# Kernel optimization log

Hardware: AMD Instinct MI355X
Metric: run time of the kernel (lower is better)

## Reference

```python
import jax, jax.numpy as jnp
import numpy as np

B, IN, H = 8192, 1024, 1024


def setup_inputs() -> dict:
    key = jax.random.key(0)
    ks = jax.random.split(key, 20)
    std = 1.0 / np.sqrt(H)
    u = lambda k, shape: jax.random.uniform(k, shape, jnp.float32, -std, std)
    inp = {
        "x": jax.random.normal(ks[0], (B, IN), jnp.float32),
        "hx": jax.random.normal(ks[1], (B, H), jnp.float32),
        "cx": jax.random.normal(ks[2], (B, H), jnp.float32),
        "task_id": 0,
        # x2h weights [H, IN] (torch Linear layout) and biases [H]
        "wxi": u(ks[3], (H, IN)), "bxi": u(ks[4], (H,)),
        "wxf": u(ks[5], (H, IN)), "bxf": u(ks[6], (H,)),
        "wxc": u(ks[7], (H, IN)), "bxc": u(ks[8], (H,)),
        "wxo": u(ks[9], (H, IN)), "bxo": u(ks[10], (H,)),
        # h2h weights [H, H] and biases [H]
        "whi": u(ks[11], (H, H)), "bhi": u(ks[12], (H,)),
        "whf": u(ks[13], (H, H)), "bhf": u(ks[14], (H,)),
        "whc": u(ks[15], (H, H)), "bhc": u(ks[16], (H,)),
        "who": u(ks[17], (H, H)), "bho": u(ks[18], (H,)),
    }
    return inp


def reference(x, hx, cx, task_id,
              wxi, bxi, wxf, bxf, wxc, bxc, wxo, bxo,
              whi, bhi, whf, bhf, whc, bhc, who, bho):
    # x = x.view(-1, x.size(1)) is identity for 2D input
    # gate pre-activations: Linear(x) + Linear(hx)  (torch: x @ W.T + b)
    ingate = x @ wxi.T + bxi + hx @ whi.T + bhi
    forgetgate = x @ wxf.T + bxf + hx @ whf.T + bhf
    cellgate = x @ wxc.T + bxc + hx @ whc.T + bhc
    outgate = x @ wxo.T + bxo + hx @ who.T + bho

    i = jax.nn.sigmoid(ingate)
    f = jax.nn.sigmoid(forgetgate)
    g = jnp.tanh(cellgate)
    o = jax.nn.sigmoid(outgate)

    cy = cx * f + i * g
    hy = o * jnp.tanh(cy)
    return hy, cy
```

## Files before the change

### kernel.cpp

```cpp
#include <hip/hip_runtime.h>
#include <hip/hip_bf16.h>

#define B_DIM  8192
#define IN_DIM 1024
#define H_DIM  1024
#define K_DIM  2048
#define BK     64
#define NT     (K_DIM / BK)

typedef __attribute__((ext_vector_type(8))) short bf16x8;
typedef __attribute__((ext_vector_type(4))) float f32x4;

__device__ __forceinline__ void mfma_16x16x32_bf16(f32x4& d, const bf16x8& a, const bf16x8& b) {
  asm("v_mfma_f32_16x16x32_bf16 %0, %1, %2, %0" : "+v"(d) : "v"(a), "v"(b));
}

__device__ __forceinline__ void gload16(const void* g, void* l) {
  __builtin_amdgcn_global_load_lds(
      (const __attribute__((address_space(1))) void*)g,
      (__attribute__((address_space(3))) void*)l,
      16, 0, 0);
}

__device__ __forceinline__ float fast_sigmoid(float x) {
  return 1.0f / (1.0f + __expf(-x));
}
__device__ __forceinline__ float fast_tanh(float x) {
  float e = __expf(2.0f * x);
  return 1.0f - 2.0f / (e + 1.0f);
}

__global__ __launch_bounds__(256) void pack_a_kernel(
    const float* __restrict__ x, const float* __restrict__ hx,
    __hip_bfloat16* __restrict__ A) {
  const int idx = blockIdx.x * 256 + threadIdx.x;
  const int r  = idx >> 8;
  const int kk = (idx & 255) << 3;
  const float* src = (kk < IN_DIM) ? (x + (size_t)r * IN_DIM + kk)
                                   : (hx + (size_t)r * H_DIM + (kk - IN_DIM));
  const float4 v0 = ((const float4*)src)[0];
  const float4 v1 = ((const float4*)src)[1];
  __hip_bfloat16 t[8];
  t[0] = __float2bfloat16(v0.x); t[1] = __float2bfloat16(v0.y);
  t[2] = __float2bfloat16(v0.z); t[3] = __float2bfloat16(v0.w);
  t[4] = __float2bfloat16(v1.x); t[5] = __float2bfloat16(v1.y);
  t[6] = __float2bfloat16(v1.z); t[7] = __float2bfloat16(v1.w);
  *(uint4*)(A + ((size_t)idx << 3)) = *(const uint4*)t;
}

__global__ __launch_bounds__(256) void pack_w_kernel(
    const float* __restrict__ wxi, const float* __restrict__ wxf,
    const float* __restrict__ wxc, const float* __restrict__ wxo,
    const float* __restrict__ whi, const float* __restrict__ whf,
    const float* __restrict__ whc, const float* __restrict__ who,
    __hip_bfloat16* __restrict__ W) {
  const int idx = blockIdx.x * 256 + threadIdx.x;
  const int row = idx >> 8;
  const int kk  = (idx & 255) << 3;
  const int g = row >> 10, n = row & 1023;
  const float* src;
  if (kk < IN_DIM) {
    const float* p = (g == 0) ? wxi : (g == 1) ? wxf : (g == 2) ? wxc : wxo;
    src = p + (size_t)n * IN_DIM + kk;
  } else {
    const float* p = (g == 0) ? whi : (g == 1) ? whf : (g == 2) ? whc : who;
    src = p + (size_t)n * H_DIM + (kk - IN_DIM);
  }
  const float4 v0 = ((const float4*)src)[0];
  const float4 v1 = ((const float4*)src)[1];
  __hip_bfloat16 t[8];
  t[0] = __float2bfloat16(v0.x); t[1] = __float2bfloat16(v0.y);
  t[2] = __float2bfloat16(v0.z); t[3] = __float2bfloat16(v0.w);
  t[4] = __float2bfloat16(v1.x); t[5] = __float2bfloat16(v1.y);
  t[6] = __float2bfloat16(v1.z); t[7] = __float2bfloat16(v1.w);
  *(uint4*)(W + ((size_t)idx << 3)) = *(const uint4*)t;
}

__global__ __launch_bounds__(512, 2) void lstm_gemm_kernel(
    const __hip_bfloat16* __restrict__ A,
    const __hip_bfloat16* __restrict__ W,
    const float* __restrict__ cx,
    const float* __restrict__ bxi, const float* __restrict__ bhi,
    const float* __restrict__ bxf, const float* __restrict__ bhf,
    const float* __restrict__ bxc, const float* __restrict__ bhc,
    const float* __restrict__ bxo, const float* __restrict__ bho,
    float* __restrict__ hy, float* __restrict__ cy) {

  __shared__ __align__(16) char lds[2][64 * 1024];

  const int tid  = threadIdx.x;
  const int w    = tid >> 6;
  const int lane = tid & 63;
  const int wm = w >> 2, wn = w & 3;
  const int lq = lane >> 4, lr16 = lane & 15;

  const int bid = blockIdx.x;
  const int xcd = bid & 7, idx = bid >> 3;
  const int col_tile = xcd * 2 + (idx >> 5);
  const int row_tile = idx & 31;
  const int row0 = row_tile * 256;
  const int col0 = col_tile * 64;

  const int srow = tid >> 3;
  const int scs  = (tid & 7) ^ (srow & 7);
  const __hip_bfloat16* Asrc = A + (size_t)(row0 + srow) * K_DIM + scs * 8;
  const __hip_bfloat16* Wsrc = W + (size_t)(col0 + srow) * K_DIM + scs * 8;
  const size_t Wg = (size_t)H_DIM * K_DIM;

  const int xr = lr16 & 7;
  const int aoff0 = wm * 16384 + lr16 * 128 + ((lq)     ^ xr) * 16;
  const int aoff1 = wm * 16384 + lr16 * 128 + ((4 + lq) ^ xr) * 16;
  const int woff0 = 32768 + (wn * 16 + lr16) * 128 + ((lq)     ^ xr) * 16;
  const int woff1 = 32768 + (wn * 16 + lr16) * 128 + ((4 + lq) ^ xr) * 16;

  f32x4 acc[4][8];
#pragma unroll
  for (int g = 0; g < 4; ++g)
#pragma unroll
    for (int m = 0; m < 8; ++m)
      acc[g][m] = (f32x4){0.f, 0.f, 0.f, 0.f};

#define STAGE_A(Q, KT)                                                        \
  {                                                                           \
    const size_t kof = (size_t)(KT) * BK;                                     \
    gload16(Asrc + kof,                 &lds[Q][tid * 16]);                   \
    gload16(Asrc + 64 * K_DIM + kof,    &lds[Q][8192  + tid * 16]);           \
    gload16(Asrc + 128 * K_DIM + kof,   &lds[Q][16384 + tid * 16]);           \
    gload16(Asrc + 192 * K_DIM + kof,   &lds[Q][24576 + tid * 16]);           \
  }
#define STAGE_W(Q, KT)                                                        \
  {                                                                           \
    const size_t kof = (size_t)(KT) * BK;                                     \
    gload16(Wsrc + kof,          &lds[Q][32768 + tid * 16]);                  \
    gload16(Wsrc + Wg + kof,     &lds[Q][40960 + tid * 16]);                  \
    gload16(Wsrc + 2 * Wg + kof, &lds[Q][49152 + tid * 16]);                  \
    gload16(Wsrc + 3 * Wg + kof, &lds[Q][57344 + tid * 16]);                  \
  }
#define BAR()  asm volatile("s_barrier" ::: "memory")

  STAGE_A(0, 0);
  STAGE_W(0, 0);
  STAGE_A(1, 1);
  asm volatile("s_waitcnt vmcnt(4)\n\ts_barrier" ::: "memory");

  bf16x8 af[4][2], wf0[2][2], wf1[2][2];

  for (int t = 0; t < NT; ++t) {
    const int p = t & 1, q = p ^ 1;
    const int tn1 = (t + 1 < NT) ? t + 1 : NT - 1;
    const int tn2 = (t + 2 < NT) ? t + 2 : NT - 1;
    const char* rb = lds[p];

#pragma unroll
    for (int m = 0; m < 4; ++m) {
      af[m][0] = *(const bf16x8*)(rb + aoff0 + m * 2048);
      af[m][1] = *(const bf16x8*)(rb + aoff1 + m * 2048);
    }
#pragma unroll
    for (int gi = 0; gi < 2; ++gi) {
      wf0[gi][0] = *(const bf16x8*)(rb + woff0 + gi * 8192);
      wf0[gi][1] = *(const bf16x8*)(rb + woff1 + gi * 8192);
    }
    STAGE_W(q, tn1);
    BAR();
    __builtin_amdgcn_s_setprio(1);
#pragma unroll
    for (int gi = 0; gi < 2; ++gi)
#pragma unroll
      for (int m = 0; m < 4; ++m) {
        mfma_16x16x32_bf16(acc[gi][m], af[m][0], wf0[gi][0]);
        mfma_16x16x32_bf16(acc[gi][m], af[m][1], wf0[gi][1]);
      }
    __builtin_amdgcn_s_setprio(0);
    BAR();

#pragma unroll
    for (int gi = 0; gi < 2; ++gi) {
      wf1[gi][0] = *(const bf16x8*)(rb + woff0 + (2 + gi) * 8192);
      wf1[gi][1] = *(const bf16x8*)(rb + woff1 + (2 + gi) * 8192);
    }
    BAR();
    __builtin_amdgcn_s_setprio(1);
#pragma unroll
    for (int gi = 0; gi < 2; ++gi)
#pragma unroll
      for (int m = 0; m < 4; ++m) {
        mfma_16x16x32_bf16(acc[2 + gi][m], af[m][0], wf1[gi][0]);
        mfma_16x16x32_bf16(acc[2 + gi][m], af[m][1], wf1[gi][1]);
      }
    __builtin_amdgcn_s_setprio(0);
    BAR();

#pragma unroll
    for (int m = 0; m < 4; ++m) {
      af[m][0] = *(const bf16x8*)(rb + aoff0 + 8192 + m * 2048);
      af[m][1] = *(const bf16x8*)(rb + aoff1 + 8192 + m * 2048);
    }
    BAR();
    __builtin_amdgcn_s_setprio(1);
#pragma unroll
    for (int gi = 0; gi < 2; ++gi)
#pragma unroll
      for (int m = 0; m < 4; ++m) {
        mfma_16x16x32_bf16(acc[2 + gi][4 + m], af[m][0], wf1[gi][0]);
        mfma_16x16x32_bf16(acc[2 + gi][4 + m], af[m][1], wf1[gi][1]);
      }
    __builtin_amdgcn_s_setprio(0);
    BAR();

    STAGE_A(p, tn2);
    asm volatile("s_waitcnt vmcnt(4)\n\ts_barrier" ::: "memory");
    __builtin_amdgcn_s_setprio(1);
#pragma unroll
    for (int gi = 0; gi < 2; ++gi)
#pragma unroll
      for (int m = 0; m < 4; ++m) {
        mfma_16x16x32_bf16(acc[gi][4 + m], af[m][0], wf0[gi][0]);
        mfma_16x16x32_bf16(acc[gi][4 + m], af[m][1], wf0[gi][1]);
      }
    __builtin_amdgcn_s_setprio(0);
    BAR();
  }

  asm volatile("s_waitcnt vmcnt(0)" ::: "memory");

  const int h = col0 + wn * 16 + lr16;
  const float bi  = bxi[h] + bhi[h];
  const float bff = bxf[h] + bhf[h];
  const float bc  = bxc[h] + bhc[h];
  const float bo  = bxo[h] + bho[h];
#pragma unroll
  for (int m = 0; m < 8; ++m) {
#pragma unroll
    for (int j = 0; j < 4; ++j) {
      const int r = row0 + wm * 128 + m * 16 + lq * 4 + j;
      const size_t o = (size_t)r * H_DIM + h;
      const float ig = fast_sigmoid(acc[0][m][j] + bi);
      const float fg = fast_sigmoid(acc[1][m][j] + bff);
      const float gg = fast_tanh   (acc[2][m][j] + bc);
      const float og = fast_sigmoid(acc[3][m][j] + bo);
      const float c  = cx[o] * fg + ig * gg;
      cy[o] = c;
      hy[o] = og * fast_tanh(c);
    }
  }
#undef STAGE_A
#undef STAGE_W
#undef BAR
}

extern "C" void kernel_launch(void* const* d_in, const int* in_sizes, int n_in,
                              void* d_out, int out_size, void* d_ws, size_t ws_size,
                              hipStream_t stream) {
  const float* x   = (const float*)d_in[0];
  const float* hx  = (const float*)d_in[1];
  const float* cx  = (const float*)d_in[2];
  const float* wxi = (const float*)d_in[4];  const float* bxi = (const float*)d_in[5];
  const float* wxf = (const float*)d_in[6];  const float* bxf = (const float*)d_in[7];
  const float* wxc = (const float*)d_in[8];  const float* bxc = (const float*)d_in[9];
  const float* wxo = (const float*)d_in[10]; const float* bxo = (const float*)d_in[11];
  const float* whi = (const float*)d_in[12]; const float* bhi = (const float*)d_in[13];
  const float* whf = (const float*)d_in[14]; const float* bhf = (const float*)d_in[15];
  const float* whc = (const float*)d_in[16]; const float* bhc = (const float*)d_in[17];
  const float* who = (const float*)d_in[18]; const float* bho = (const float*)d_in[19];

  __hip_bfloat16* Abf = (__hip_bfloat16*)d_ws;
  __hip_bfloat16* Wbf = (__hip_bfloat16*)((char*)d_ws + (size_t)B_DIM * K_DIM * 2);

  float* hy  = (float*)d_out;
  float* cyo = (float*)d_out + (size_t)B_DIM * H_DIM;

  pack_a_kernel<<<(B_DIM * K_DIM / 8) / 256, 256, 0, stream>>>(x, hx, Abf);
  pack_w_kernel<<<(4 * H_DIM * K_DIM / 8) / 256, 256, 0, stream>>>(
      wxi, wxf, wxc, wxo, whi, whf, whc, who, Wbf);

  lstm_gemm_kernel<<<dim3(512), 512, 0, stream>>>(
      Abf, Wbf, cx, bxi, bhi, bxf, bhf, bxc, bhc, bxo, bho, hy, cyo);
}
```

Measured before the change: 169.8 us.

## Restructure GEMM main loop into register-prefetched pipeline with fewer barriers

```diff
diff --git a/kernel.cpp b/kernel.cpp
--- a/kernel.cpp
+++ b/kernel.cpp
@@ -12,7 +12,7 @@
 typedef __attribute__((ext_vector_type(4))) float f32x4;
 
 __device__ __forceinline__ void mfma_16x16x32_bf16(f32x4& d, const bf16x8& a, const bf16x8& b) {
-  asm("v_mfma_f32_16x16x32_bf16 %0, %1, %2, %0" : "+v"(d) : "v"(a), "v"(b));
+  asm volatile("v_mfma_f32_16x16x32_bf16 %0, %1, %2, %0" : "+v"(d) : "v"(a), "v"(b));
 }
 
 __device__ __forceinline__ void gload16(const void* g, void* l) {
@@ -95,11 +95,8 @@
   const int lq = lane >> 4, lr16 = lane & 15;
 
   const int bid = blockIdx.x;
-  const int xcd = bid & 7, idx = bid >> 3;
-  const int col_tile = xcd * 2 + (idx >> 5);
-  const int row_tile = idx & 31;
-  const int row0 = row_tile * 256;
-  const int col0 = col_tile * 64;
+  const int row0 = (bid & 31) * 256;
+  const int col0 = (bid >> 5) * 64;
 
   const int srow = tid >> 3;
   const int scs  = (tid & 7) ^ (srow & 7);
@@ -123,10 +120,10 @@
 #define STAGE_A(Q, KT)                                                        \
   {                                                                           \
     const size_t kof = (size_t)(KT) * BK;                                     \
-    gload16(Asrc + kof,                 &lds[Q][tid * 16]);                   \
-    gload16(Asrc + 64 * K_DIM + kof,    &lds[Q][8192  + tid * 16]);           \
-    gload16(Asrc + 128 * K_DIM + kof,   &lds[Q][16384 + tid * 16]);           \
-    gload16(Asrc + 192 * K_DIM + kof,   &lds[Q][24576 + tid * 16]);           \
+    gload16(Asrc + kof,               &lds[Q][tid * 16]);                     \
+    gload16(Asrc + 64 * K_DIM + kof,  &lds[Q][8192  + tid * 16]);             \
+    gload16(Asrc + 128 * K_DIM + kof, &lds[Q][16384 + tid * 16]);             \
+    gload16(Asrc + 192 * K_DIM + kof, &lds[Q][24576 + tid * 16]);             \
   }
 #define STAGE_W(Q, KT)                                                        \
   {                                                                           \
@@ -136,93 +133,96 @@
     gload16(Wsrc + 2 * Wg + kof, &lds[Q][49152 + tid * 16]);                  \
     gload16(Wsrc + 3 * Wg + kof, &lds[Q][57344 + tid * 16]);                  \
   }
-#define BAR()  asm volatile("s_barrier" ::: "memory")
 
   STAGE_A(0, 0);
   STAGE_W(0, 0);
-  STAGE_A(1, 1);
-  asm volatile("s_waitcnt vmcnt(4)\n\ts_barrier" ::: "memory");
-
-  bf16x8 af[4][2], wf0[2][2], wf1[2][2];
+  asm volatile("s_waitcnt vmcnt(0)\n\ts_barrier" ::: "memory");
+
+  bf16x8 af0[4][2], af1[4][2], wf01[2][2], wf23[2][2];
+  {
+    const char* rb = lds[0];
+#pragma unroll
+    for (int m = 0; m < 4; ++m) {
+      af0[m][0] = *(const bf16x8*)(rb + aoff0 + m * 2048);
+      af0[m][1] = *(const bf16x8*)(rb + aoff1 + m * 2048);
+    }
+#pragma unroll
+    for (int gi = 0; gi < 2; ++gi) {
+      wf01[gi][0] = *(const bf16x8*)(rb + woff0 + gi * 8192);
+      wf01[gi][1] = *(const bf16x8*)(rb + woff1 + gi * 8192);
+    }
+  }
 
   for (int t = 0; t < NT; ++t) {
     const int p = t & 1, q = p ^ 1;
     const int tn1 = (t + 1 < NT) ? t + 1 : NT - 1;
-    const int tn2 = (t + 2 < NT) ? t + 2 : NT - 1;
     const char* rb = lds[p];
+    const char* nb = lds[q];
+
+#pragma unroll
+    for (int gi = 0; gi < 2; ++gi) {
+      wf23[gi][0] = *(const bf16x8*)(rb + woff0 + (2 + gi) * 8192);
+      wf23[gi][1] = *(const bf16x8*)(rb + woff1 + (2 + gi) * 8192);
+    }
+    STAGE_A(q, tn1);
+    STAGE_W(q, tn1);
+    __builtin_amdgcn_s_setprio(1);
+#pragma unroll
+    for (int gi = 0; gi < 2; ++gi)
+#pragma unroll
+      for (int m = 0; m < 4; ++m) {
+        mfma_16x16x32_bf16(acc[gi][m], af0[m][0], wf01[gi][0]);
+        mfma_16x16x32_bf16(acc[gi][m], af0[m][1], wf01[gi][1]);
+      }
+    __builtin_amdgcn_s_setprio(0);
 
 #pragma unroll
     for (int m = 0; m < 4; ++m) {
-      af[m][0] = *(const bf16x8*)(rb + aoff0 + m * 2048);
-      af[m][1] = *(const bf16x8*)(rb + aoff1 + m * 2048);
+      af1[m][0] = *(const bf16x8*)(rb + aoff0 + 8192 + m * 2048);
+      af1[m][1] = *(const bf16x8*)(rb + aoff1 + 8192 + m * 2048);
+    }
+    __builtin_amdgcn_s_setprio(1);
+#pragma unroll
+    for (int gi = 0; gi < 2; ++gi)
+#pragma unroll
+      for (int m = 0; m < 4; ++m) {
+        mfma_16x16x32_bf16(acc[2 + gi][m], af0[m][0], wf23[gi][0]);
+        mfma_16x16x32_bf16(acc[2 + gi][m], af0[m][1], wf23[gi][1]);
+      }
+    __builtin_amdgcn_s_setprio(0);
+
+    __builtin_amdgcn_s_setprio(1);
+#pragma unroll
+    for (int gi = 0; gi < 2; ++gi)
+#pragma unroll
+      for (int m = 0; m < 4; ++m) {
+        mfma_16x16x32_bf16(acc[gi][4 + m], af1[m][0], wf01[gi][0]);
+        mfma_16x16x32_bf16(acc[gi][4 + m], af1[m][1], wf01[gi][1]);
+      }
+    __builtin_amdgcn_s_setprio(0);
+
+    asm volatile("s_waitcnt vmcnt(0)\n\ts_barrier" ::: "memory");
+#pragma unroll
+    for (int m = 0; m < 4; ++m) {
+      af0[m][0] = *(const bf16x8*)(nb + aoff0 + m * 2048);
+      af0[m][1] = *(const bf16x8*)(nb + aoff1 + m * 2048);
     }
 #pragma unroll
     for (int gi = 0; gi < 2; ++gi) {
-      wf0[gi][0] = *(const bf16x8*)(rb + woff0 + gi * 8192);
-      wf0[gi][1] = *(const bf16x8*)(rb + woff1 + gi * 8192);
-    }
-    STAGE_W(q, tn1);
-    BAR();
-    __builtin_amdgcn_s_setprio(1);
-#pragma unroll
-    for (int gi = 0; gi < 2; ++gi)
-#pragma unroll
-      for (int m = 0; m < 4; ++m) {
-        mfma_16x16x32_bf16(acc[gi][m], af[m][0], wf0[gi][0]);
-        mfma_16x16x32_bf16(acc[gi][m], af[m][1], wf0[gi][1]);
-      }
-    __builtin_amdgcn_s_setprio(0);
-    BAR();
-
-#pragma unroll
-    for (int gi = 0; gi < 2; ++gi) {
-      wf1[gi][0] = *(const bf16x8*)(rb + woff0 + (2 + gi) * 8192);
-      wf1[gi][1] = *(const bf16x8*)(rb + woff1 + (2 + gi) * 8192);
-    }
-    BAR();
-    __builtin_amdgcn_s_setprio(1);
-#pragma unroll
-    for (int gi = 0; gi < 2; ++gi)
-#pragma unroll
-      for (int m = 0; m < 4; ++m) {
-        mfma_16x16x32_bf16(acc[2 + gi][m], af[m][0], wf1[gi][0]);
-        mfma_16x16x32_bf16(acc[2 + gi][m], af[m][1], wf1[gi][1]);
-      }
-    __builtin_amdgcn_s_setprio(0);
-    BAR();
-
-#pragma unroll
-    for (int m = 0; m < 4; ++m) {
-      af[m][0] = *(const bf16x8*)(rb + aoff0 + 8192 + m * 2048);
-      af[m][1] = *(const bf16x8*)(rb + aoff1 + 8192 + m * 2048);
-    }
-    BAR();
-    __builtin_amdgcn_s_setprio(1);
-#pragma unroll
-    for (int gi = 0; gi < 2; ++gi)
-#pragma unroll
-      for (int m = 0; m < 4; ++m) {
-        mfma_16x16x32_bf16(acc[2 + gi][4 + m], af[m][0], wf1[gi][0]);
-        mfma_16x16x32_bf16(acc[2 + gi][4 + m], af[m][1], wf1[gi][1]);
-      }
-    __builtin_amdgcn_s_setprio(0);
-    BAR();
-
-    STAGE_A(p, tn2);
-    asm volatile("s_waitcnt vmcnt(4)\n\ts_barrier" ::: "memory");
-    __builtin_amdgcn_s_setprio(1);
-#pragma unroll
-    for (int gi = 0; gi < 2; ++gi)
-#pragma unroll
-      for (int m = 0; m < 4; ++m) {
-        mfma_16x16x32_bf16(acc[gi][4 + m], af[m][0], wf0[gi][0]);
-        mfma_16x16x32_bf16(acc[gi][4 + m], af[m][1], wf0[gi][1]);
-      }
-    __builtin_amdgcn_s_setprio(0);
-    BAR();
-  }
-
-  asm volatile("s_waitcnt vmcnt(0)" ::: "memory");
+      wf01[gi][0] = *(const bf16x8*)(nb + woff0 + gi * 8192);
+      wf01[gi][1] = *(const bf16x8*)(nb + woff1 + gi * 8192);
+    }
+    __builtin_amdgcn_s_setprio(1);
+#pragma unroll
+    for (int gi = 0; gi < 2; ++gi)
+#pragma unroll
+      for (int m = 0; m < 4; ++m) {
+        mfma_16x16x32_bf16(acc[2 + gi][4 + m], af1[m][0], wf23[gi][0]);
+        mfma_16x16x32_bf16(acc[2 + gi][4 + m], af1[m][1], wf23[gi][1]);
+      }
+    __builtin_amdgcn_s_setprio(0);
+    asm volatile("s_barrier" ::: "memory");
+  }
 
   const int h = col0 + wn * 16 + lr16;
   const float bi  = bxi[h] + bhi[h];
@@ -246,7 +246,6 @@
   }
 #undef STAGE_A
 #undef STAGE_W
-#undef BAR
 }
 
 extern "C" void kernel_launch(void* const* d_in, const int* in_sizes, int n_in,
```

Result: faster. 163.8 us (-3.5%).
